# Kernel optimization log

Hardware: AMD Instinct MI355X
Metric: run time of the kernel (lower is better)

## Reference

```python
import jax, jax.numpy as jnp
import numpy as np

B, N, DIN, DOUT, CHEB_K, EMBED = 64, 2048, 64, 64, 3, 16


def setup_inputs() -> dict:
    key = jax.random.key(0)
    k0, k1, k2, k3 = jax.random.split(key, 4)
    return {
        "x": jax.random.normal(k0, (B, N, DIN), dtype=jnp.float32),
        "node_embeddings": jax.random.normal(k1, (N, EMBED), dtype=jnp.float32),
        "weights_pool": jax.random.normal(k2, (EMBED, CHEB_K, DIN, DOUT), dtype=jnp.float32) * 0.02,
        "bias_pool": jax.random.normal(k3, (EMBED, DOUT), dtype=jnp.float32) * 0.02,
    }


def reference(x, node_embeddings, weights_pool, bias_pool):
    # x: (B, N, dim_in); node_embeddings: (N, embed_dim)
    n = node_embeddings.shape[0]
    # adaptive adjacency: softmax(relu(E E^T)) row-wise
    supports = jax.nn.softmax(jax.nn.relu(node_embeddings @ node_embeddings.T), axis=1)
    # Chebyshev polynomial basis: T0=I, T1=S, Tk = 2 S T_{k-1} - T_{k-2}
    tk = [jnp.eye(n, dtype=x.dtype), supports]
    for _ in range(2, CHEB_K):
        tk.append(2.0 * supports @ tk[-1] - tk[-2])
    S = jnp.stack(tk, axis=0)  # (K, N, N)
    # per-node weights/bias generated from embeddings
    weights = jnp.einsum('nd,dkio->nkio', node_embeddings, weights_pool)  # (N,K,din,dout)
    bias = node_embeddings @ bias_pool  # (N, dout)
    # graph conv: aggregate over neighbors for each Chebyshev order
    x_g = jnp.einsum('knm,bmc->bnkc', S, x)  # (B, N, K, din)
    out = jnp.einsum('bnki,nkio->bno', x_g, weights) + bias  # (B, N, dout)
    return out
```

## Files before the change

### kernel.cpp

```cpp
#include <hip/hip_runtime.h>
#include <hip/hip_bf16.h>

typedef unsigned short u16;
typedef short short8 __attribute__((ext_vector_type(8)));
typedef short short4v __attribute__((ext_vector_type(4)));
typedef float floatx4 __attribute__((ext_vector_type(4)));

#define NNODES 2048
#define BATCH  64
#define DIN    64
#define DOUT   64
#define EMB    16

__device__ __forceinline__ u16 f2bf(float f) {
  union { float f; unsigned u; } v; v.f = f;
  unsigned r = v.u + 0x7fffu + ((v.u >> 16) & 1u);
  return (u16)(r >> 16);
}

__device__ __forceinline__ void gload_lds16(const void* g, void* l) {
  __builtin_amdgcn_global_load_lds(
      (const __attribute__((address_space(1))) void*)g,
      (__attribute__((address_space(3))) void*)l, 16, 0, 0);
}

__global__ __launch_bounds__(256) void prologue(const float* __restrict__ E,
                                                const float* __restrict__ pool,
                                                const float* __restrict__ x,
                                                u16* __restrict__ Sb,
                                                u16* __restrict__ xtt,
                                                float* __restrict__ peff) {
  int bid = blockIdx.x;
  int t = threadIdx.x;

  if (bid < 2048) {
    int n = bid;
    const float4* ep = (const float4*)(E + (size_t)n * EMB);
    float4 e0 = ep[0], e1 = ep[1], e2 = ep[2], e3 = ep[3];
    float lg[8];
    float mx = 0.0f;
#pragma unroll
    for (int j = 0; j < 8; j++) {
      int m = t + j * 256;
      const float4* mp = (const float4*)(E + (size_t)m * EMB);
      float4 a = mp[0], b = mp[1], c = mp[2], d = mp[3];
      float dot = e0.x * a.x + e0.y * a.y + e0.z * a.z + e0.w * a.w
                + e1.x * b.x + e1.y * b.y + e1.z * b.z + e1.w * b.w
                + e2.x * c.x + e2.y * c.y + e2.z * c.z + e2.w * c.w
                + e3.x * d.x + e3.y * d.y + e3.z * d.z + e3.w * d.w;
      dot = fmaxf(dot, 0.0f);
      lg[j] = dot;
      mx = fmaxf(mx, dot);
    }
    __shared__ float smax[4], ssum[4];
#pragma unroll
    for (int off = 32; off > 0; off >>= 1) mx = fmaxf(mx, __shfl_xor(mx, off, 64));
    if ((t & 63) == 0) smax[t >> 6] = mx;
    __syncthreads();
    mx = fmaxf(fmaxf(smax[0], smax[1]), fmaxf(smax[2], smax[3]));
    float sum = 0.0f;
#pragma unroll
    for (int j = 0; j < 8; j++) {
      float e = __expf(lg[j] - mx);
      lg[j] = e;
      sum += e;
    }
#pragma unroll
    for (int off = 32; off > 0; off >>= 1) sum += __shfl_xor(sum, off, 64);
    if ((t & 63) == 0) ssum[t >> 6] = sum;
    __syncthreads();
    sum = ssum[0] + ssum[1] + ssum[2] + ssum[3];
    float inv = 1.0f / sum;
#pragma unroll
    for (int j = 0; j < 8; j++)
      Sb[(size_t)n * NNODES + t + j * 256] = f2bf(lg[j] * inv);

  } else if (bid < 4096) {
    __shared__ float tile[64][68];
    int u = bid - 2048;
    int b = u >> 5;
    int m0 = (u & 31) * 64;
    int r = t >> 2, cs = (t & 3) * 16;
    const float* xp = x + ((size_t)b * NNODES + m0 + r) * DIN + cs;
    float4 v0 = ((const float4*)xp)[0];
    float4 v1 = ((const float4*)xp)[1];
    float4 v2 = ((const float4*)xp)[2];
    float4 v3 = ((const float4*)xp)[3];
    *(float4*)&tile[r][cs]      = v0;
    *(float4*)&tile[r][cs + 4]  = v1;
    *(float4*)&tile[r][cs + 8]  = v2;
    *(float4*)&tile[r][cs + 12] = v3;
    __syncthreads();
    int c = t >> 2, ms = (t & 3) * 16;
    short8 o0, o1;
#pragma unroll
    for (int j = 0; j < 8; j++) o0[j] = (short)f2bf(tile[ms + j][c]);
#pragma unroll
    for (int j = 0; j < 8; j++) o1[j] = (short)f2bf(tile[ms + 8 + j][c]);
    u16* op = xtt + ((size_t)b * 64 + c) * NNODES + m0 + ms;
    *(short8*)op = o0;
    *(short8*)(op + 8) = o1;

  } else {
    int idx = (bid - 4096) * 256 + t;
    int d = idx / 12288;
    int r = idx - d * 12288;
    int o = r / 192;
    int ki = r - o * 192;
    int k = ki >> 6, i = ki & 63;
    float p = pool[(size_t)d * 12288 + k * 4096 + i * 64 + o];
    if (k == 0) p -= pool[(size_t)d * 12288 + 8192 + i * 64 + o];
    if (k == 2) p += p;
    peff[idx] = p;
  }
}

__global__ __launch_bounds__(256) void wgen2(const float* __restrict__ E,
                                             const float* __restrict__ peff,
                                             u16* __restrict__ W) {
  __shared__ float Es[128][17];
  int t = threadIdx.x;
  int n0 = blockIdx.y * 128;
  for (int idx = t; idx < 128 * EMB; idx += 256)
    Es[idx >> 4][idx & 15] = E[(size_t)n0 * EMB + idx];
  int e = blockIdx.x * 256 + t;
  float pv[16];
#pragma unroll
  for (int d = 0; d < 16; d++) pv[d] = peff[(size_t)d * 12288 + e];
  __syncthreads();
#pragma unroll 4
  for (int nn = 0; nn < 128; nn++) {
    float acc = 0.0f;
#pragma unroll
    for (int d = 0; d < 16; d++) acc = fmaf(Es[nn][d], pv[d], acc);
    W[(size_t)(n0 + nn) * 12288 + e] = f2bf(acc);
  }
}

#define GK 2048
#define GN 4096
#define NT 32
#define BUFU 24576

#define GEMM_PREAMBLE                                                          \
  __shared__ u16 smem[3 * BUFU];                                               \
  int t = threadIdx.x, lane = t & 63, wave = t >> 6;                           \
  int lin = blockIdx.y * gridDim.x + blockIdx.x;                               \
  int nwg = gridDim.x * gridDim.y;                                             \
  int sw = (lin & 7) * (nwg >> 3) + (lin >> 3);                                \
  int bx = sw & 31, by = sw >> 5;                                              \
  int m0 = by * 256, n0 = bx * 128;                                            \
  const u16* pg[6];                                                            \
  int lof[6];                                                                  \
  _Pragma("unroll") for (int j = 0; j < 4; j++) {                              \
    int c = t + 512 * j;                                                       \
    int row = c >> 3;                                                          \
    int gs = (c & 7) ^ (row & 7);                                              \
    pg[j] = A + (size_t)(m0 + row) * GK + gs * 8;                              \
    lof[j] = c * 8;                                                            \
  }                                                                            \
  _Pragma("unroll") for (int j = 0; j < 2; j++) {                              \
    int c = t + 512 * j;                                                       \
    int row = c >> 3;                                                          \
    int gs = (c & 7) ^ (row & 7);                                              \
    pg[4 + j] = Bt + (size_t)(n0 + row) * GK + gs * 8;                         \
    lof[4 + j] = 16384 + c * 8;                                                \
  }                                                                            \
  auto stage = [&](int b, int kt) {                                            \
    _Pragma("unroll") for (int j = 0; j < 6; j++)                              \
        gload_lds16(pg[j] + kt, &smem[b * BUFU + lof[j]]);                     \
  };                                                                           \
  int wr = wave >> 1, wc = wave & 1;                                           \
  int lr = lane & 15, lg = lane >> 4;                                          \
  floatx4 acc[4][4];                                                           \
  _Pragma("unroll") for (int mi = 0; mi < 4; mi++)                             \
      _Pragma("unroll") for (int ni = 0; ni < 4; ni++)                         \
          acc[mi][ni] = (floatx4)0.0f;                                         \
  int aoff[2][4], boff[2][4];                                                  \
  _Pragma("unroll") for (int s = 0; s < 2; s++) {                              \
    _Pragma("unroll") for (int mi = 0; mi < 4; mi++) {                         \
      int row = wr * 64 + mi * 16 + lr;                                        \
      int slot = s * 4 + lg;                                                   \
      aoff[s][mi] = row * 64 + (slot ^ (row & 7)) * 8;                         \
    }                                                                          \
    _Pragma("unroll") for (int ni = 0; ni < 4; ni++) {                         \
      int row = wc * 64 + ni * 16 + lr;                                        \
      int slot = s * 4 + lg;                                                   \
      boff[s][ni] = 16384 + row * 64 + (slot ^ (row & 7)) * 8;                 \
    }                                                                          \
  }                                                                            \
  auto compute = [&](int b) {                                                  \
    const u16* base = &smem[b * BUFU];                                         \
    short8 af[2][4], bf[2][4];                                                 \
    _Pragma("unroll") for (int s = 0; s < 2; s++) {                            \
      _Pragma("unroll") for (int mi = 0; mi < 4; mi++)                         \
          af[s][mi] = *(const short8*)(base + aoff[s][mi]);                    \
      _Pragma("unroll") for (int ni = 0; ni < 4; ni++)                         \
          bf[s][ni] = *(const short8*)(base + boff[s][ni]);                    \
    }                                                                          \
    _Pragma("unroll") for (int s = 0; s < 2; s++)                              \
        _Pragma("unroll") for (int mi = 0; mi < 4; mi++)                       \
            _Pragma("unroll") for (int ni = 0; ni < 4; ni++)                   \
                acc[mi][ni] = __builtin_amdgcn_mfma_f32_16x16x32_bf16(         \
                    af[s][mi], bf[s][ni], acc[mi][ni], 0, 0, 0);               \
  };                                                                           \
  stage(0, 0);                                                                 \
  stage(1, 64);                                                                \
  for (int tt = 0; tt < NT - 2; ++tt) {                                        \
    asm volatile("s_waitcnt vmcnt(6)" ::: "memory");                           \
    __builtin_amdgcn_s_barrier();                                              \
    stage((tt + 2) % 3, (tt + 2) * 64);                                        \
    compute(tt % 3);                                                           \
  }                                                                            \
  asm volatile("s_waitcnt vmcnt(6)" ::: "memory");                             \
  __builtin_amdgcn_s_barrier();                                                \
  compute((NT - 2) % 3);                                                       \
  asm volatile("s_waitcnt vmcnt(0)" ::: "memory");                             \
  __builtin_amdgcn_s_barrier();                                                \
  compute((NT - 1) % 3);                                                       \
  _Pragma("unroll") for (int mi = 0; mi < 4; mi++)                             \
      _Pragma("unroll") for (int ni = 0; ni < 4; ni++) {                       \
    int row = m0 + wr * 64 + mi * 16 + lg * 4;                                 \
    int col = n0 + wc * 64 + ni * 16 + lr;                                     \
    _Pragma("unroll") for (int r = 0; r < 4; r++)                              \
        C[(size_t)(row + r) * GN + col] = f2bf(acc[mi][ni][r]);                \
  }

__global__ __launch_bounds__(512) void gemm_plain(const u16* __restrict__ A,
                                                  const u16* __restrict__ Bt,
                                                  u16* __restrict__ C) {
  GEMM_PREAMBLE
}

__global__ __launch_bounds__(512) void gemm_tr(const u16* __restrict__ A,
                                               const u16* __restrict__ Bt,
                                               u16* __restrict__ C,
                                               u16* __restrict__ Ct) {
  GEMM_PREAMBLE
  __syncthreads();
  u16* scr = smem + wave * 4096;
#pragma unroll
  for (int mi = 0; mi < 4; mi++)
#pragma unroll
    for (int ni = 0; ni < 4; ni++) {
      int ncol = ni * 16 + lr;
      int chunk = mi * 2 + (lg >> 1);
      int off = ncol * 64 + ((chunk ^ (ncol & 7)) << 3) + (lg & 1) * 4;
      short4v sv;
#pragma unroll
      for (int r = 0; r < 4; r++) sv[r] = (short)f2bf(acc[mi][ni][r]);
      *(short4v*)&scr[off] = sv;
    }
  int c = lane;
  u16* op = Ct + (size_t)(n0 + wc * 64 + c) * GK + m0 + wr * 64;
#pragma unroll
  for (int jj = 0; jj < 8; jj++) {
    short8 v = *(const short8*)&scr[c * 64 + ((jj ^ (c & 7)) << 3)];
    *(short8*)(op + jj * 8) = v;
  }
}

__global__ __launch_bounds__(256) void final_k(const float* __restrict__ x,
                                               const float* __restrict__ E,
                                               const float* __restrict__ bpool,
                                               const u16* __restrict__ xg1,
                                               const u16* __restrict__ xg2,
                                               const u16* __restrict__ W,
                                               float* __restrict__ out) {
  __shared__ u16 Xs[3][64][72];
  __shared__ u16 Ws[64][200];
  __shared__ float bias_s[64];
  int n = blockIdx.x, t = threadIdx.x;

  {
    int b = t >> 2, i0 = (t & 3) * 16;
    const float* xp = x + ((size_t)b * NNODES + n) * DIN + i0;
    float4 v0 = ((const float4*)xp)[0];
    float4 v1 = ((const float4*)xp)[1];
    float4 v2 = ((const float4*)xp)[2];
    float4 v3 = ((const float4*)xp)[3];
    u16* d = &Xs[0][b][i0];
    d[0] = f2bf(v0.x); d[1] = f2bf(v0.y); d[2] = f2bf(v0.z); d[3] = f2bf(v0.w);
    d[4] = f2bf(v1.x); d[5] = f2bf(v1.y); d[6] = f2bf(v1.z); d[7] = f2bf(v1.w);
    d[8] = f2bf(v2.x); d[9] = f2bf(v2.y); d[10] = f2bf(v2.z); d[11] = f2bf(v2.w);
    d[12] = f2bf(v3.x); d[13] = f2bf(v3.y); d[14] = f2bf(v3.z); d[15] = f2bf(v3.w);
  }
  for (int idx = t; idx < 512; idx += 256) {
    short8 v1 = *(const short8*)(xg1 + (size_t)n * 4096 + idx * 8);
    *(short8*)&Xs[1][idx >> 3][(idx & 7) * 8] = v1;
    short8 v2 = *(const short8*)(xg2 + (size_t)n * 4096 + idx * 8);
    *(short8*)&Xs[2][idx >> 3][(idx & 7) * 8] = v2;
  }
  for (int idx = t; idx < 1536; idx += 256) {
    short8 v = *(const short8*)(W + (size_t)n * 12288 + idx * 8);
    int o = idx / 24, w8 = idx - o * 24;
    *(short8*)&Ws[o][w8 * 8] = v;
  }
  if (t < 64) {
    float acc = 0.0f;
#pragma unroll
    for (int d = 0; d < 16; d++)
      acc = fmaf(E[(size_t)n * EMB + d], bpool[d * 64 + t], acc);
    bias_s[t] = acc;
  }
  __syncthreads();

  int lane = t & 63, wave = t >> 6;
  int lr = lane & 15, lg = lane >> 4;
  int wb = wave * 16;
  floatx4 acc[4];
#pragma unroll
  for (int ot = 0; ot < 4; ot++) acc[ot] = (floatx4)0.0f;

#pragma unroll
  for (int ks = 0; ks < 6; ks++) {
    int kk = ks * 32 + lg * 8;
    short8 a = *(const short8*)&Xs[kk >> 6][wb + lr][kk & 63];
#pragma unroll
    for (int ot = 0; ot < 4; ot++) {
      short8 bb = *(const short8*)&Ws[ot * 16 + lr][kk];
      acc[ot] = __builtin_amdgcn_mfma_f32_16x16x32_bf16(a, bb, acc[ot], 0, 0, 0);
    }
  }
#pragma unroll
  for (int ot = 0; ot < 4; ot++) {
    int o = ot * 16 + lr;
    float bs = bias_s[o];
#pragma unroll
    for (int r = 0; r < 4; r++) {
      int b = wb + lg * 4 + r;
      out[((size_t)b * NNODES + n) * DOUT + o] = acc[ot][r] + bs;
    }
  }
}

extern "C" void kernel_launch(void* const* d_in, const int* in_sizes, int n_in,
                              void* d_out, int out_size, void* d_ws, size_t ws_size,
                              hipStream_t stream) {
  const float* x     = (const float*)d_in[0];
  const float* E     = (const float*)d_in[1];
  const float* pool  = (const float*)d_in[2];
  const float* bpool = (const float*)d_in[3];
  float* out = (float*)d_out;

  char* ws = (char*)d_ws;
  u16* Sb   = (u16*)(ws);
  u16* xtt  = (u16*)(ws + 8388608);
  u16* xg1  = (u16*)(ws + 25165824);
  u16* xg1t = (u16*)(ws + 41943040);
  u16* xg2  = (u16*)(ws + 58720256);
  u16* Wall = (u16*)(ws + 75497472);
  float* peff = (float*)(ws + 58720256);

  prologue<<<4864, 256, 0, stream>>>(E, pool, x, Sb, xtt, peff);
  wgen2<<<dim3(48, NNODES / 128), 256, 0, stream>>>(E, peff, Wall);
  gemm_tr<<<dim3(32, 8), 512, 0, stream>>>(Sb, xtt, xg1, xg1t);
  gemm_plain<<<dim3(32, 8), 512, 0, stream>>>(Sb, xg1t, xg2);
  final_k<<<NNODES, 256, 0, stream>>>(x, E, bpool, xg1, xg2, Wall, out);
}
```

Before: 163.4 us.

## Fuse weight generation into prologue and re-layout W with swizzled LDS transpose

Per-node weight generation now runs as extra blocks inside the prologue kernel. The effective Chebyshev pool (T0−T2 fold and doubling) is computed on the fly from the original pool layout, which removes the separate wgen2 launch and the peff round trip through global memory. W is now stored in the natural [k,i,o] order, and final_k transposes it into an XOR-swizzled LDS tile using scalar 16-bit stores. Separately, gemm_tr's transpose scratch switches from an XOR swizzle to a padded row stride of 72. The tradeoffs are more, narrower LDS writes in final_k and a heavier, longer-running first branch of the prologue.

```diff
diff --git a/kernel.cpp b/kernel.cpp
--- a/kernel.cpp
+++ b/kernel.cpp
@@ -29,12 +29,36 @@
                                                 const float* __restrict__ x,
                                                 u16* __restrict__ Sb,
                                                 u16* __restrict__ xtt,
-                                                float* __restrict__ peff) {
+                                                u16* __restrict__ W) {
   int bid = blockIdx.x;
   int t = threadIdx.x;
 
-  if (bid < 2048) {
-    int n = bid;
+  if (bid < 768) {
+    __shared__ float Es[128][17];
+    int ec = bid % 48, nc = bid / 48;
+    int e = ec * 256 + t;
+    int n0 = nc * 128;
+    for (int idx = t; idx < 128 * EMB; idx += 256)
+      Es[idx >> 4][idx & 15] = E[(size_t)n0 * EMB + idx];
+    float pv[16];
+#pragma unroll
+    for (int d = 0; d < 16; d++) {
+      float p = pool[(size_t)d * 12288 + e];
+      if (e < 4096) p -= pool[(size_t)d * 12288 + 8192 + e];
+      if (e >= 8192) p += p;
+      pv[d] = p;
+    }
+    __syncthreads();
+#pragma unroll 4
+    for (int nn = 0; nn < 128; nn++) {
+      float acc = 0.0f;
+#pragma unroll
+      for (int d = 0; d < 16; d++) acc = fmaf(Es[nn][d], pv[d], acc);
+      W[(size_t)(n0 + nn) * 12288 + e] = f2bf(acc);
+    }
+
+  } else if (bid < 2816) {
+    int n = bid - 768;
     const float4* ep = (const float4*)(E + (size_t)n * EMB);
     float4 e0 = ep[0], e1 = ep[1], e2 = ep[2], e3 = ep[3];
     float lg[8];
@@ -75,9 +99,9 @@
     for (int j = 0; j < 8; j++)
       Sb[(size_t)n * NNODES + t + j * 256] = f2bf(lg[j] * inv);
 
-  } else if (bid < 4096) {
+  } else {
     __shared__ float tile[64][68];
-    int u = bid - 2048;
+    int u = bid - 2816;
     int b = u >> 5;
     int m0 = (u & 31) * 64;
     int r = t >> 2, cs = (t & 3) * 16;
@@ -100,40 +124,6 @@
     u16* op = xtt + ((size_t)b * 64 + c) * NNODES + m0 + ms;
     *(short8*)op = o0;
     *(short8*)(op + 8) = o1;
-
-  } else {
-    int idx = (bid - 4096) * 256 + t;
-    int d = idx / 12288;
-    int r = idx - d * 12288;
-    int o = r / 192;
-    int ki = r - o * 192;
-    int k = ki >> 6, i = ki & 63;
-    float p = pool[(size_t)d * 12288 + k * 4096 + i * 64 + o];
-    if (k == 0) p -= pool[(size_t)d * 12288 + 8192 + i * 64 + o];
-    if (k == 2) p += p;
-    peff[idx] = p;
-  }
-}
-
-__global__ __launch_bounds__(256) void wgen2(const float* __restrict__ E,
-                                             const float* __restrict__ peff,
-                                             u16* __restrict__ W) {
-  __shared__ float Es[128][17];
-  int t = threadIdx.x;
-  int n0 = blockIdx.y * 128;
-  for (int idx = t; idx < 128 * EMB; idx += 256)
-    Es[idx >> 4][idx & 15] = E[(size_t)n0 * EMB + idx];
-  int e = blockIdx.x * 256 + t;
-  float pv[16];
-#pragma unroll
-  for (int d = 0; d < 16; d++) pv[d] = peff[(size_t)d * 12288 + e];
-  __syncthreads();
-#pragma unroll 4
-  for (int nn = 0; nn < 128; nn++) {
-    float acc = 0.0f;
-#pragma unroll
-    for (int d = 0; d < 16; d++) acc = fmaf(Es[nn][d], pv[d], acc);
-    W[(size_t)(n0 + nn) * 12288 + e] = f2bf(acc);
   }
 }
 
@@ -238,14 +228,14 @@
                                                u16* __restrict__ Ct) {
   GEMM_PREAMBLE
   __syncthreads();
-  u16* scr = smem + wave * 4096;
+  u16* scr = smem + wave * 4608;
 #pragma unroll
   for (int mi = 0; mi < 4; mi++)
 #pragma unroll
     for (int ni = 0; ni < 4; ni++) {
       int ncol = ni * 16 + lr;
       int chunk = mi * 2 + (lg >> 1);
-      int off = ncol * 64 + ((chunk ^ (ncol & 7)) << 3) + (lg & 1) * 4;
+      int off = ncol * 72 + chunk * 8 + (lg & 1) * 4;
       short4v sv;
 #pragma unroll
       for (int r = 0; r < 4; r++) sv[r] = (short)f2bf(acc[mi][ni][r]);
@@ -255,7 +245,7 @@
   u16* op = Ct + (size_t)(n0 + wc * 64 + c) * GK + m0 + wr * 64;
 #pragma unroll
   for (int jj = 0; jj < 8; jj++) {
-    short8 v = *(const short8*)&scr[c * 64 + ((jj ^ (c & 7)) << 3)];
+    short8 v = *(const short8*)&scr[c * 72 + jj * 8];
     *(short8*)(op + jj * 8) = v;
   }
 }
@@ -268,7 +258,7 @@
                                                const u16* __restrict__ W,
                                                float* __restrict__ out) {
   __shared__ u16 Xs[3][64][72];
-  __shared__ u16 Ws[64][200];
+  __shared__ u16 Ws[64 * 200];
   __shared__ float bias_s[64];
   int n = blockIdx.x, t = threadIdx.x;
 
@@ -293,8 +283,14 @@
   }
   for (int idx = t; idx < 1536; idx += 256) {
     short8 v = *(const short8*)(W + (size_t)n * 12288 + idx * 8);
-    int o = idx / 24, w8 = idx - o * 24;
-    *(short8*)&Ws[o][w8 * 8] = v;
+    int kk = idx >> 3;
+    int oo = (idx & 7) * 8;
+    int c8 = kk >> 3, k7 = kk & 7;
+#pragma unroll
+    for (int j = 0; j < 8; j++) {
+      int o = oo + j;
+      Ws[o * 200 + ((c8 ^ (o >> 3)) << 3) + k7] = (u16)v[j];
+    }
   }
   if (t < 64) {
     float acc = 0.0f;
@@ -315,10 +311,12 @@
 #pragma unroll
   for (int ks = 0; ks < 6; ks++) {
     int kk = ks * 32 + lg * 8;
+    int c8 = ks * 4 + lg;
     short8 a = *(const short8*)&Xs[kk >> 6][wb + lr][kk & 63];
 #pragma unroll
     for (int ot = 0; ot < 4; ot++) {
-      short8 bb = *(const short8*)&Ws[ot * 16 + lr][kk];
+      int o = ot * 16 + lr;
+      short8 bb = *(const short8*)&Ws[o * 200 + ((c8 ^ (o >> 3)) << 3)];
       acc[ot] = __builtin_amdgcn_mfma_f32_16x16x32_bf16(a, bb, acc[ot], 0, 0, 0);
     }
   }
@@ -350,10 +348,8 @@
   u16* xg1t = (u16*)(ws + 41943040);
   u16* xg2  = (u16*)(ws + 58720256);
   u16* Wall = (u16*)(ws + 75497472);
-  float* peff = (float*)(ws + 58720256);
-
-  prologue<<<4864, 256, 0, stream>>>(E, pool, x, Sb, xtt, peff);
-  wgen2<<<dim3(48, NNODES / 128), 256, 0, stream>>>(E, peff, Wall);
+
+  prologue<<<4864, 256, 0, stream>>>(E, pool, x, Sb, xtt, Wall);
   gemm_tr<<<dim3(32, 8), 512, 0, stream>>>(Sb, xtt, xg1, xg1t);
   gemm_plain<<<dim3(32, 8), 512, 0, stream>>>(Sb, xg1t, xg2);
   final_k<<<NNODES, 256, 0, stream>>>(x, E, bpool, xg1, xg2, Wall, out);
```

Result: faster. 154.7 us (-5.3%).
